# Optimization experiments

Measured on AMD Instinct MI355X. Metric: run time of the kernel, lower is better.

The kernel has to match this reference:

```python
import jax, jax.numpy as jnp
import numpy as np

PART_INDICES = [[0, 1, 2, 3, 4], [5, 6, 11, 12], [5, 7, 9], [6, 8, 10], [11, 12, 13, 14, 15, 16]]
B, J, D_IN, D_H, D_OUT = 4096, 25, 512, 256, 512


def _xavier(key, shape):
    fan_in, fan_out = shape
    lim = float(np.sqrt(6.0 / (fan_in + fan_out)))
    return jax.random.uniform(key, shape, jnp.float32, -lim, lim)


def setup_inputs() -> dict:
    key = jax.random.key(0)
    ks = list(jax.random.split(key, 64))
    it = iter(ks)
    inp = {}
    inp["x"] = jax.random.normal(next(it), (B, J, D_IN), jnp.float32)
    inp["adj_global"] = jax.random.uniform(next(it), (J, J), jnp.float32)
    for p, idx in enumerate(PART_INDICES):
        n = len(idx)
        inp[f"adj_local_{p}"] = jax.random.uniform(next(it), (n, n), jnp.float32)
    # global GCN params (2 layers)
    inp["Wg0"] = _xavier(next(it), (D_IN, D_H)); inp["bg0"] = jnp.zeros((D_H,), jnp.float32)
    inp["Wg1"] = _xavier(next(it), (D_H, D_OUT)); inp["bg1"] = jnp.zeros((D_OUT,), jnp.float32)
    # local GCN params (5 parts x 2 layers)
    for p in range(5):
        inp[f"Wl{p}a"] = _xavier(next(it), (D_IN, D_H)); inp[f"bl{p}a"] = jnp.zeros((D_H,), jnp.float32)
        inp[f"Wl{p}b"] = _xavier(next(it), (D_H, D_OUT)); inp[f"bl{p}b"] = jnp.zeros((D_OUT,), jnp.float32)
    # fusion MLP: Linear(2*D_OUT, D_OUT) -> ReLU -> Linear(D_OUT, D_OUT)
    inp["Wf0"] = _xavier(next(it), (2 * D_OUT, D_OUT)); inp["bf0"] = jnp.zeros((D_OUT,), jnp.float32)
    inp["Wf1"] = _xavier(next(it), (D_OUT, D_OUT)); inp["bf1"] = jnp.zeros((D_OUT,), jnp.float32)
    return inp


def _gcn(x, adj, W, b):
    # symmetric degree normalization D^-1/2 A D^-1/2, then (norm_adj @ (x @ W)) + b
    d = jnp.clip(adj.sum(axis=1), 1e-6, None) ** -0.5
    norm_adj = d[:, None] * adj * d[None, :]                       # [n, n]
    return jnp.einsum('ij,bjf->bif', norm_adj, x @ W) + b          # [B, n, out]


def reference(x, adj_global, adj_local_0, adj_local_1, adj_local_2, adj_local_3, adj_local_4,
              Wg0, bg0, Wg1, bg1,
              Wl0a, bl0a, Wl0b, bl0b,
              Wl1a, bl1a, Wl1b, bl1b,
              Wl2a, bl2a, Wl2b, bl2b,
              Wl3a, bl3a, Wl3b, bl3b,
              Wl4a, bl4a, Wl4b, bl4b,
              Wf0, bf0, Wf1, bf1):
    adjs = [adj_local_0, adj_local_1, adj_local_2, adj_local_3, adj_local_4]
    lps = [(Wl0a, bl0a, Wl0b, bl0b), (Wl1a, bl1a, Wl1b, bl1b), (Wl2a, bl2a, Wl2b, bl2b),
           (Wl3a, bl3a, Wl3b, bl3b), (Wl4a, bl4a, Wl4b, bl4b)]
    # global branch
    xg = jax.nn.relu(_gcn(x, adj_global, Wg0, bg0))
    xg = jax.nn.relu(_gcn(xg, adj_global, Wg1, bg1))
    # local branch: scatter per-part outputs back (later parts overwrite overlaps, like torch)
    xl = jnp.zeros((x.shape[0], x.shape[1], D_OUT), x.dtype)
    for p, idx in enumerate(PART_INDICES):
        Wa, ba, Wb, bb = lps[p]
        idx_a = jnp.asarray(idx)
        xp = x[:, idx_a]                                           # [B, n_p, D_IN]
        xp = jax.nn.relu(_gcn(xp, adjs[p], Wa, ba))
        xp = jax.nn.relu(_gcn(xp, adjs[p], Wb, bb))
        xl = xl.at[:, idx_a].set(xp)
    # fusion MLP
    xc = jnp.concatenate([xg, xl], axis=-1)                        # [B, J, 2*D_OUT]
    return jax.nn.relu(xc @ Wf0 + bf0) @ Wf1 + bf1                 # [B, J, D_OUT]
```

## Files before the change

kernel.cpp:

```cpp
#include <hip/hip_runtime.h>


#define BATCH 4096
#define NJOINT 25
#define MROWS (BATCH * NJOINT)
#define SZ_FULL (MROWS * 512)

typedef __attribute__((ext_vector_type(8))) short short8;
typedef __attribute__((ext_vector_type(4))) float float4_;

__device__ __forceinline__ float b2f(ushort u) {
    union { float f; uint32_t i; } x; x.i = ((uint32_t)u) << 16; return x.f;
}
__device__ __forceinline__ ushort f2b(float f) {
    union { float f; uint32_t i; } x; x.f = f;
    uint32_t r = x.i + 0x7fff + ((x.i >> 16) & 1);
    return (ushort)(r >> 16);
}
__device__ __forceinline__ void async16(const void* g, void* l) {
    __builtin_amdgcn_global_load_lds(
        (const __attribute__((address_space(1))) void*)g,
        (__attribute__((address_space(3))) void*)l, 16, 0, 0);
}

__device__ void norm_one(const float* A, int n, float* out, float* sAdj, float* sD) {
    int t = threadIdx.x;
    for (int i = t; i < n * n; i += 256) sAdj[i] = A[i];
    __syncthreads();
    if (t < n) {
        float s = 0.f;
        for (int j = 0; j < n; j++) s += sAdj[t * n + j];
        sD[t] = 1.0f / sqrtf(fmaxf(s, 1e-6f));
    }
    __syncthreads();
    for (int i = t; i < n * n; i += 256) {
        int r = i / n, c = i % n;
        out[i] = sD[r] * sAdj[i] * sD[c];
    }
    __syncthreads();
}

__global__ __launch_bounds__(256) void adjnorm_kernel(
    const float* Ag, const float* A0, const float* A2, const float* A3,
    const float* A4, float* ADJ) {
    __shared__ float sAdj[640];
    __shared__ float sD[32];
    norm_one(Ag, 25, ADJ, sAdj, sD);
    norm_one(A0, 5, ADJ + 640 + 0 * 64, sAdj, sD);
    norm_one(A2, 3, ADJ + 640 + 1 * 64, sAdj, sD);
    norm_one(A3, 3, ADJ + 640 + 2 * 64, sAdj, sD);
    norm_one(A4, 6, ADJ + 640 + 3 * 64, sAdj, sD);
}

__global__ __launch_bounds__(256) void cvt_bf16(const float* __restrict__ in,
                                                ushort* __restrict__ out, int n4) {
    int id = blockIdx.x * 256 + threadIdx.x;
    if (id < n4) {
        float4 v = ((const float4*)in)[id];
        ushort4 o;
        o.x = f2b(v.x); o.y = f2b(v.y); o.z = f2b(v.z); o.w = f2b(v.w);
        ((ushort4*)out)[id] = o;
    }
}

struct WDesc { const float* W; ushort* Wt; int K, N, nxlog, end; };
struct WParams { WDesc d[12]; };

__global__ __launch_bounds__(256) void wtrans_all(WParams P) {
    __shared__ float tile[32][33];
    int bid = blockIdx.x;
    int i = 0, start = 0;
    while (bid >= P.d[i].end) { start = P.d[i].end; i++; }
    const WDesc& D = P.d[i];
    int local = bid - start;
    int bx = local & ((1 << D.nxlog) - 1);
    int by = local >> D.nxlog;
    int K = D.K, N = D.N;
    int t = threadIdx.x, tx = t & 31, ty = t >> 5;
    int k0 = by * 32, n0 = bx * 32;
    for (int r = ty; r < 32; r += 8)
        tile[r][tx] = D.W[(size_t)(k0 + r) * N + n0 + tx];
    __syncthreads();
    for (int r = ty; r < 32; r += 8)
        D.Wt[(size_t)(n0 + r) * K + k0 + tx] = f2b(tile[tx][r]);
}

__global__ __launch_bounds__(256) void zero_tail(ushort* __restrict__ XGL) {
    int id = blockIdx.x * 256 + threadIdx.x;
    int f4 = id & 127;
    int rj = (id >> 7) & 7;
    int b = id >> 10;
    ushort4 z; z.x = 0; z.y = 0; z.z = 0; z.w = 0;
    ((ushort4*)(XGL + ((size_t)(b * 25 + 17 + rj) * 1024 + 512)))[f4] = z;
}

struct GDesc {
    const ushort* A; const ushort* Wt; const float* bias; void* C;
    int K, lda, ldc, nTiles, wgEnd, gn, flags, pad;
    int gmap[6];
};
struct GParams { GDesc g[5]; };

__global__ __launch_bounds__(512, 2) void gemmg(GParams P) {
    __shared__ ushort lds[65536];
    int t = threadIdx.x;
    int l = t & 63, w = t >> 6;

    int nwg = (int)gridDim.x;
    int cpx = nwg >> 3;
    int wg = ((int)blockIdx.x & 7) * cpx + ((int)blockIdx.x >> 3);

    int gi = 0, wg0 = 0;
    while (wg >= P.g[gi].wgEnd) { wg0 = P.g[gi].wgEnd; gi++; }
    const GDesc& G = P.g[gi];
    int lw = wg - wg0;
    int tm, tn;
    if (G.nTiles == 2) { tm = lw >> 1; tn = lw & 1; }
    else               { tm = lw;      tn = 0; }
    int bm = tm << 8, bn = tn << 8;
    const int K = G.K, lda = G.lda, ldc = G.ldc;
    const bool GATHER = (G.flags & 1) != 0;
    const bool BIAS   = (G.flags & 2) != 0;
    const bool RELU   = (G.flags & 4) != 0;
    const bool OUTF32 = (G.flags & 8) != 0;

    int srow = (w << 4) + (l >> 3);
    int sch = ((l & 7) ^ (l >> 3)) << 3;
    const ushort* pA[2][2];
    const ushort* pB[2][2];
#pragma unroll
    for (int h = 0; h < 2; h++)
#pragma unroll
        for (int i = 0; i < 2; i++) {
            int r = bm + h * 128 + srow + i * 8;
            if (GATHER) { int b = r / G.gn; r = b * 25 + G.gmap[r - b * G.gn]; }
            pA[h][i] = G.A + (size_t)r * lda + sch;
            int c = bn + h * 128 + srow + i * 8;
            pB[h][i] = G.Wt + (size_t)c * K + sch;
        }
    int stga = w << 10;

    int wm = w >> 2, wn = w & 3;
    int lr = l & 15, q = l >> 4;
    int cx = lr & 7;
    int ca0 = (q ^ cx) << 3;
    int ca1 = ca0 ^ 32;
    int ra = (wm << 13) + (lr << 6);
    int rb = 16384 + ((wn >> 1) << 13) + ((wn & 1) << 12) + (lr << 6);

    float4_ acc[8][4];
#pragma unroll
    for (int fi = 0; fi < 8; fi++)
#pragma unroll
        for (int fj = 0; fj < 4; fj++) acc[fi][fj] = (float4_)0.f;
    short8 bfr[4][2];

#define FENCE() asm volatile("" ::: "memory")
#define STG_A(DB, H, KT) do {                                              \
        async16(pA[H][0] + (KT) * 64, &lds[(DB) + (H) * 8192 + stga]);     \
        async16(pA[H][1] + (KT) * 64, &lds[(DB) + (H) * 8192 + stga + 512]); \
    } while (0)
#define STG_B(DB, H, KT) do {                                              \
        async16(pB[H][0] + (KT) * 64, &lds[(DB) + 16384 + (H) * 8192 + stga]); \
        async16(pB[H][1] + (KT) * 64, &lds[(DB) + 16384 + (H) * 8192 + stga + 512]); \
    } while (0)

#define DO_PHASE(DB, FI0, RDB, WAITST, STMT) do {                          \
        short8 af00, af01, af10, af11;                                     \
        if (RDB) {                                                         \
            _Pragma("unroll")                                              \
            for (int fj = 0; fj < 4; fj++) {                               \
                bfr[fj][0] = *(const short8*)&lds[(DB) + rb + fj * 1024 + ca0]; \
                bfr[fj][1] = *(const short8*)&lds[(DB) + rb + fj * 1024 + ca1]; \
            }                                                              \
        }                                                                  \
        af00 = *(const short8*)&lds[(DB) + ra + (FI0) * 1024 + ca0];       \
        af01 = *(const short8*)&lds[(DB) + ra + (FI0) * 1024 + ca1];       \
        af10 = *(const short8*)&lds[(DB) + ra + ((FI0) + 1) * 1024 + ca0]; \
        af11 = *(const short8*)&lds[(DB) + ra + ((FI0) + 1) * 1024 + ca1]; \
        STMT                                                               \
        WAITST                                                             \
        __builtin_amdgcn_s_barrier();                                      \
        FENCE();                                                           \
        __builtin_amdgcn_s_setprio(1);                                     \
        _Pragma("unroll")                                                  \
        for (int fj = 0; fj < 4; fj++) {                                   \
            acc[FI0][fj] = __builtin_amdgcn_mfma_f32_16x16x32_bf16(        \
                af00, bfr[fj][0], acc[FI0][fj], 0, 0, 0);                  \
            acc[FI0][fj] = __builtin_amdgcn_mfma_f32_16x16x32_bf16(        \
                af01, bfr[fj][1], acc[FI0][fj], 0, 0, 0);                  \
            acc[(FI0) + 1][fj] = __builtin_amdgcn_mfma_f32_16x16x32_bf16(  \
                af10, bfr[fj][0], acc[(FI0) + 1][fj], 0, 0, 0);            \
            acc[(FI0) + 1][fj] = __builtin_amdgcn_mfma_f32_16x16x32_bf16(  \
                af11, bfr[fj][1], acc[(FI0) + 1][fj], 0, 0, 0);            \
        }                                                                  \
        __builtin_amdgcn_s_setprio(0);                                     \
        __builtin_amdgcn_s_barrier();                                      \
        FENCE();                                                           \
    } while (0)

    int NT = K >> 6;
    int NITER = NT >> 1;

    STG_A(0, 0, 0); STG_A(0, 1, 0);
    STG_B(0, 0, 0); STG_B(0, 1, 0);
    STG_B(32768, 0, 1); STG_B(32768, 1, 1);
    asm volatile("s_waitcnt vmcnt(4)" ::: "memory");
    __builtin_amdgcn_s_barrier();
    FENCE();

    for (int j = 0; j < NITER; ++j) {
        int k1 = 2 * j + 1, k2 = 2 * j + 2, k3 = 2 * j + 3;
        bool nl = (j + 1 < NITER);
        DO_PHASE(0, 0, true, , STG_A(32768, 0, k1););
        DO_PHASE(0, 2, false, , STG_A(32768, 1, k1););
        DO_PHASE(0, 4, false, , if (nl) STG_B(0, 0, k2););
        DO_PHASE(0, 6, false,
                 if (nl) { asm volatile("s_waitcnt vmcnt(4)" ::: "memory"); }
                 else    { asm volatile("s_waitcnt vmcnt(0)" ::: "memory"); },
                 if (nl) STG_B(0, 1, k2););
        DO_PHASE(32768, 0, true, , if (nl) STG_A(0, 0, k2););
        DO_PHASE(32768, 2, false, , if (nl) STG_A(0, 1, k2););
        DO_PHASE(32768, 4, false, , if (nl) STG_B(32768, 0, k3););
        DO_PHASE(32768, 6, false,
                 if (nl) { asm volatile("s_waitcnt vmcnt(4)" ::: "memory"); },
                 if (nl) STG_B(32768, 1, k3););
    }
#undef DO_PHASE
#undef STG_A
#undef STG_B
#undef FENCE

    int cl = lr;
    float bv[4];
#pragma unroll
    for (int fj = 0; fj < 4; fj++)
        bv[fj] = BIAS ? G.bias[bn + (wn << 6) + (fj << 4) + cl] : 0.f;
#pragma unroll
    for (int fi = 0; fi < 8; fi++) {
        int row0 = bm + (wm << 7) + (fi << 4) + (q << 2);
#pragma unroll
        for (int r = 0; r < 4; r++) {
            size_t rowoff = (size_t)(row0 + r) * ldc;
#pragma unroll
            for (int fj = 0; fj < 4; fj++) {
                int col = bn + (wn << 6) + (fj << 4) + cl;
                float v = acc[fi][fj][r] + bv[fj];
                if (RELU) v = fmaxf(v, 0.f);
                if (OUTF32)
                    ((float*)G.C)[rowoff + col] = v;
                else
                    ((ushort*)G.C)[rowoff + col] = f2b(v);
            }
        }
    }
}

struct M1Desc { ushort* T; const float* adj; const float* bias; int nj; };
struct M1Params { M1Desc d[5]; };

template <int NJ>
__device__ __forceinline__ void mix1_body(ushort* base, const float* As, float bi) {
    float v[NJ];
#pragma unroll
    for (int j = 0; j < NJ; j++) v[j] = b2f(base[(size_t)j * 256]);
#pragma unroll
    for (int i = 0; i < NJ; i++) {
        float o = 0.f;
#pragma unroll
        for (int j = 0; j < NJ; j++) o += As[i * NJ + j] * v[j];
        base[(size_t)i * 256] = f2b(fmaxf(o + bi, 0.f));
    }
}

__global__ __launch_bounds__(256) void mixg1(M1Params P) {
    __shared__ float As[625];
    int r = blockIdx.x >> 12;
    const M1Desc& D = P.d[r];
    int t = threadIdx.x;
    int nj = D.nj;
    for (int i = t; i < nj * nj; i += 256) As[i] = D.adj[i];
    __syncthreads();
    int id = ((blockIdx.x & 4095) << 8) + t;
    int f = id & 255, b = id >> 8;
    ushort* base = D.T + ((size_t)b * nj) * 256 + f;
    float bi = D.bias[f];
    switch (nj) {
        case 25: mix1_body<25>(base, As, bi); break;
        case 5:  mix1_body<5>(base, As, bi); break;
        case 3:  mix1_body<3>(base, As, bi); break;
        default: mix1_body<6>(base, As, bi); break;
    }
}

struct M2Desc {
    const ushort* src; ushort* dst; const float* adj; const float* bias;
    int nj, sldr; int jm[25];
};
struct M2Params { M2Desc d[5]; };

template <int NJ>
__device__ __forceinline__ void mix2_body(const ushort* src, int sldr, ushort* dst,
                                          const int* jms, const float* As, float bi) {
    float v[NJ];
#pragma unroll
    for (int j = 0; j < NJ; j++) v[j] = b2f(src[(size_t)j * sldr]);
#pragma unroll
    for (int i = 0; i < NJ; i++) {
        float o = 0.f;
#pragma unroll
        for (int j = 0; j < NJ; j++) o += As[i * NJ + j] * v[j];
        dst[(size_t)jms[i] * 1024] = f2b(fmaxf(o + bi, 0.f));
    }
}

__global__ __launch_bounds__(256) void mixg2(M2Params P) {
    __shared__ float As[625];
    __shared__ int jms[25];
    int r = blockIdx.x >> 13;
    const M2Desc& D = P.d[r];
    int t = threadIdx.x;
    int nj = D.nj;
    for (int i = t; i < nj * nj; i += 256) As[i] = D.adj[i];
    if (t < nj) jms[t] = D.jm[t];
    __syncthreads();
    int id = ((blockIdx.x & 8191) << 8) + t;
    int f = id & 511, b = id >> 9;
    const ushort* src = D.src + ((size_t)b * nj) * D.sldr + f;
    ushort* dst = D.dst + (size_t)b * 25 * 1024 + f;
    float bi = D.bias[f];
    switch (nj) {
        case 25: mix2_body<25>(src, D.sldr, dst, jms, As, bi); break;
        case 5:  mix2_body<5>(src, D.sldr, dst, jms, As, bi); break;
        case 3:  mix2_body<3>(src, D.sldr, dst, jms, As, bi); break;
        default: mix2_body<6>(src, D.sldr, dst, jms, As, bi); break;
    }
}

extern "C" void kernel_launch(void* const* d_in, const int* in_sizes, int n_in,
                              void* d_out, int out_size, void* d_ws,
                              size_t ws_size, hipStream_t stream) {
    const float* x    = (const float*)d_in[0];
    const float* adjg = (const float*)d_in[1];
    const float* al0  = (const float*)d_in[2];
    const float* al2  = (const float*)d_in[4];
    const float* al3  = (const float*)d_in[5];
    const float* al4  = (const float*)d_in[6];
    const float* Wg0  = (const float*)d_in[7];
    const float* bg0  = (const float*)d_in[8];
    const float* Wg1  = (const float*)d_in[9];
    const float* bg1  = (const float*)d_in[10];
    const float* Wf0  = (const float*)d_in[31];
    const float* bf0  = (const float*)d_in[32];
    const float* Wf1  = (const float*)d_in[33];
    const float* bf1  = (const float*)d_in[34];

    float* ws = (float*)d_ws;
    float* ADJ = ws;
    ushort* U   = (ushort*)(ws + 4096);
    ushort* Xb  = U;
    ushort* XGL = Xb + (size_t)SZ_FULL;
    ushort* T   = XGL + (size_t)MROWS * 1024;
    ushort* P1  = T + (size_t)MROWS * 256;
    ushort* Wb  = P1 + (size_t)BATCH * 17 * 256;
    ushort* P3  = Xb;
    ushort* HF  = Xb;

    ushort* Wg0t = Wb;
    ushort* Wg1t = Wb + 131072;
    ushort* Wf0t = Wb + 262144;
    ushort* Wf1t = Wb + 786432;
    ushort* Wpt  = Wb + 1048576;

    struct Part { int n, widx; int idx[6]; };
    const Part parts[4] = {
        {5, 11, {0, 1, 2, 3, 4, 0}},
        {3, 19, {5, 7, 9, 0, 0, 0}},
        {3, 23, {6, 8, 10, 0, 0, 0}},
        {6, 27, {11, 12, 13, 14, 15, 16}},
    };
    const int cumn[4] = {0, 5, 8, 11};

    dim3 blk(256), blk512(512);

    adjnorm_kernel<<<1, blk, 0, stream>>>(adjg, al0, al2, al3, al4, ADJ);
    cvt_bf16<<<SZ_FULL / 4 / 256, blk, 0, stream>>>(x, Xb, SZ_FULL / 4);
    zero_tail<<<16384, blk, 0, stream>>>(XGL);

    {
        WParams WP{};
        int e = 0, i = 0;
        auto add = [&](const float* W, ushort* Wt, int K, int N) {
            int nx = N >> 5;
            int nxlog = (nx == 8) ? 3 : ((nx == 16) ? 4 : 5);
            e += nx * (K >> 5);
            WP.d[i++] = {W, Wt, K, N, nxlog, e};
        };
        add(Wg0, Wg0t, 512, 256);
        add(Wg1, Wg1t, 256, 512);
        add(Wf0, Wf0t, 1024, 512);
        add(Wf1, Wf1t, 512, 512);
        for (int qv = 0; qv < 4; qv++) {
            add((const float*)d_in[parts[qv].widx], Wpt + qv * 262144, 512, 256);
            add((const float*)d_in[parts[qv].widx + 2], Wpt + qv * 262144 + 131072, 256, 512);
        }
        wtrans_all<<<2048, blk, 0, stream>>>(WP);
    }

    auto setg = [](GDesc& g, const ushort* A, const ushort* Wt, const float* bias,
                   void* C, int K, int lda, int ldc, int nT, int wgEnd, int gn,
                   int flags, const int* map) {
        g.A = A; g.Wt = Wt; g.bias = bias; g.C = C; g.K = K; g.lda = lda;
        g.ldc = ldc; g.nTiles = nT; g.wgEnd = wgEnd; g.gn = gn; g.flags = flags;
        g.pad = 0;
        for (int i = 0; i < 6; i++) g.gmap[i] = map ? map[i] : 0;
    };

    {
        GParams GA{};
        int e = 400;
        setg(GA.g[0], Xb, Wg0t, nullptr, T, 512, 512, 256, 1, e, 0, 0, nullptr);
        for (int qv = 0; qv < 4; qv++) {
            e += parts[qv].n * 16;
            setg(GA.g[1 + qv], Xb, Wpt + qv * 262144, nullptr,
                 P1 + (size_t)BATCH * cumn[qv] * 256,
                 512, 512, 256, 1, e, parts[qv].n, 1, parts[qv].idx);
        }
        gemmg<<<672, blk512, 0, stream>>>(GA);
    }

    {
        M1Params M1{};
        M1.d[0] = {T, ADJ, bg0, 25};
        for (int qv = 0; qv < 4; qv++)
            M1.d[1 + qv] = {P1 + (size_t)BATCH * cumn[qv] * 256,
                            ADJ + 640 + qv * 64,
                            (const float*)d_in[parts[qv].widx + 1],
                            parts[qv].n};
        mixg1<<<20480, blk, 0, stream>>>(M1);
    }

    {
        GParams GB{};
        int e = 800;
        setg(GB.g[0], T, Wg1t, nullptr, XGL, 256, 256, 1024, 2, e, 0, 0, nullptr);
        for (int qv = 0; qv < 4; qv++) {
            e += parts[qv].n * 32;
            setg(GB.g[1 + qv], P1 + (size_t)BATCH * cumn[qv] * 256,
                 Wpt + qv * 262144 + 131072, nullptr,
                 P3 + (size_t)BATCH * cumn[qv] * 512,
                 256, 256, 512, 2, e, 0, 0, nullptr);
        }
        gemmg<<<1344, blk512, 0, stream>>>(GB);
    }

    {
        M2Params M2{};
        M2.d[0].src = XGL; M2.d[0].dst = XGL; M2.d[0].adj = ADJ;
        M2.d[0].bias = bg1; M2.d[0].nj = 25; M2.d[0].sldr = 1024;
        for (int i = 0; i < 25; i++) M2.d[0].jm[i] = i;
        for (int qv = 0; qv < 4; qv++) {
            M2Desc& D = M2.d[1 + qv];
            D.src = P3 + (size_t)BATCH * cumn[qv] * 512;
            D.dst = XGL + 512;
            D.adj = ADJ + 640 + qv * 64;
            D.bias = (const float*)d_in[parts[qv].widx + 3];
            D.nj = parts[qv].n; D.sldr = 512;
            for (int i = 0; i < 25; i++) D.jm[i] = (i < 6) ? parts[qv].idx[i] : 0;
        }
        mixg2<<<40960, blk, 0, stream>>>(M2);
    }

    {
        GParams GF{};
        setg(GF.g[0], XGL, Wf0t, bf0, HF, 1024, 1024, 512, 2, 800, 0, 2 | 4, nullptr);
        gemmg<<<800, blk512, 0, stream>>>(GF);
    }
    {
        GParams GO{};
        setg(GO.g[0], HF, Wf1t, bf1, d_out, 512, 512, 512, 2, 800, 0, 2 | 8, nullptr);
        gemmg<<<800, blk512, 0, stream>>>(GO);
    }

    (void)in_sizes; (void)n_in; (void)out_size; (void)ws_size;
}
```

Before: 963.9 us.

## Halve GEMM pipeline phases to four per iteration with explicit lgkmcnt waits

Restructures the double-buffered MFMA main loop so each phase computes four row fragments (32 MFMAs) instead of two. The phase count per k-pair drops from eight to four, and the number of workgroup barriers falls with it. Each phase now issues four async global-to-LDS loads instead of two. Explicit lgkmcnt waits and sched_barriers replace the compiler memory fences to control where LDS reads overlap the barrier. This trades finer load/compute interleaving and some register pressure for less synchronization overhead, and the vmcnt accounting has to stay consistent with the new load grouping.

```diff
diff --git a/kernel.cpp b/kernel.cpp
--- a/kernel.cpp
+++ b/kernel.cpp
@@ -155,18 +155,21 @@
         for (int fj = 0; fj < 4; fj++) acc[fi][fj] = (float4_)0.f;
     short8 bfr[4][2];
 
-#define FENCE() asm volatile("" ::: "memory")
-#define STG_A(DB, H, KT) do {                                              \
-        async16(pA[H][0] + (KT) * 64, &lds[(DB) + (H) * 8192 + stga]);     \
-        async16(pA[H][1] + (KT) * 64, &lds[(DB) + (H) * 8192 + stga + 512]); \
+#define STG_AT(DB, KT) do {                                                \
+        async16(pA[0][0] + (KT) * 64, &lds[(DB) + stga]);                  \
+        async16(pA[0][1] + (KT) * 64, &lds[(DB) + stga + 512]);            \
+        async16(pA[1][0] + (KT) * 64, &lds[(DB) + 8192 + stga]);           \
+        async16(pA[1][1] + (KT) * 64, &lds[(DB) + 8192 + stga + 512]);     \
     } while (0)
-#define STG_B(DB, H, KT) do {                                              \
-        async16(pB[H][0] + (KT) * 64, &lds[(DB) + 16384 + (H) * 8192 + stga]); \
-        async16(pB[H][1] + (KT) * 64, &lds[(DB) + 16384 + (H) * 8192 + stga + 512]); \
+#define STG_BT(DB, KT) do {                                                \
+        async16(pB[0][0] + (KT) * 64, &lds[(DB) + 16384 + stga]);          \
+        async16(pB[0][1] + (KT) * 64, &lds[(DB) + 16384 + stga + 512]);    \
+        async16(pB[1][0] + (KT) * 64, &lds[(DB) + 24576 + stga]);          \
+        async16(pB[1][1] + (KT) * 64, &lds[(DB) + 24576 + stga + 512]);    \
     } while (0)
 
 #define DO_PHASE(DB, FI0, RDB, WAITST, STMT) do {                          \
-        short8 af00, af01, af10, af11;                                     \
+        short8 af[4][2];                                                   \
         if (RDB) {                                                         \
             _Pragma("unroll")                                              \
             for (int fj = 0; fj < 4; fj++) {                               \
@@ -174,62 +177,58 @@
                 bfr[fj][1] = *(const short8*)&lds[(DB) + rb + fj * 1024 + ca1]; \
             }                                                              \
         }                                                                  \
-        af00 = *(const short8*)&lds[(DB) + ra + (FI0) * 1024 + ca0];       \
-        af01 = *(const short8*)&lds[(DB) + ra + (FI0) * 1024 + ca1];       \
-        af10 = *(const short8*)&lds[(DB) + ra + ((FI0) + 1) * 1024 + ca0]; \
-        af11 = *(const short8*)&lds[(DB) + ra + ((FI0) + 1) * 1024 + ca1]; \
+        _Pragma("unroll")                                                  \
+        for (int fi = 0; fi < 4; fi++) {                                   \
+            af[fi][0] = *(const short8*)&lds[(DB) + ra + ((FI0) + fi) * 1024 + ca0]; \
+            af[fi][1] = *(const short8*)&lds[(DB) + ra + ((FI0) + fi) * 1024 + ca1]; \
+        }                                                                  \
         STMT                                                               \
         WAITST                                                             \
+        if (RDB) asm volatile("s_waitcnt lgkmcnt(8)");                     \
+        __builtin_amdgcn_sched_barrier(0);                                 \
         __builtin_amdgcn_s_barrier();                                      \
-        FENCE();                                                           \
+        asm volatile("s_waitcnt lgkmcnt(0)" ::: "memory");                 \
+        __builtin_amdgcn_sched_barrier(0);                                 \
         __builtin_amdgcn_s_setprio(1);                                     \
         _Pragma("unroll")                                                  \
-        for (int fj = 0; fj < 4; fj++) {                                   \
-            acc[FI0][fj] = __builtin_amdgcn_mfma_f32_16x16x32_bf16(        \
-                af00, bfr[fj][0], acc[FI0][fj], 0, 0, 0);                  \
-            acc[FI0][fj] = __builtin_amdgcn_mfma_f32_16x16x32_bf16(        \
-                af01, bfr[fj][1], acc[FI0][fj], 0, 0, 0);                  \
-            acc[(FI0) + 1][fj] = __builtin_amdgcn_mfma_f32_16x16x32_bf16(  \
-                af10, bfr[fj][0], acc[(FI0) + 1][fj], 0, 0, 0);            \
-            acc[(FI0) + 1][fj] = __builtin_amdgcn_mfma_f32_16x16x32_bf16(  \
-                af11, bfr[fj][1], acc[(FI0) + 1][fj], 0, 0, 0);            \
-        }                                                                  \
+        for (int kk = 0; kk < 2; kk++)                                     \
+            _Pragma("unroll")                                              \
+            for (int fi = 0; fi < 4; fi++)                                 \
+                _Pragma("unroll")                                          \
+                for (int fj = 0; fj < 4; fj++)                             \
+                    acc[(FI0) + fi][fj] = __builtin_amdgcn_mfma_f32_16x16x32_bf16( \
+                        af[fi][kk], bfr[fj][kk], acc[(FI0) + fi][fj], 0, 0, 0); \
         __builtin_amdgcn_s_setprio(0);                                     \
+        __builtin_amdgcn_sched_barrier(0);                                 \
         __builtin_amdgcn_s_barrier();                                      \
-        FENCE();                                                           \
     } while (0)
 
     int NT = K >> 6;
     int NITER = NT >> 1;
 
-    STG_A(0, 0, 0); STG_A(0, 1, 0);
-    STG_B(0, 0, 0); STG_B(0, 1, 0);
-    STG_B(32768, 0, 1); STG_B(32768, 1, 1);
+    STG_AT(0, 0);
+    STG_BT(0, 0);
+    STG_BT(32768, 1);
     asm volatile("s_waitcnt vmcnt(4)" ::: "memory");
+    __builtin_amdgcn_sched_barrier(0);
     __builtin_amdgcn_s_barrier();
-    FENCE();
 
     for (int j = 0; j < NITER; ++j) {
         int k1 = 2 * j + 1, k2 = 2 * j + 2, k3 = 2 * j + 3;
         bool nl = (j + 1 < NITER);
-        DO_PHASE(0, 0, true, , STG_A(32768, 0, k1););
-        DO_PHASE(0, 2, false, , STG_A(32768, 1, k1););
-        DO_PHASE(0, 4, false, , if (nl) STG_B(0, 0, k2););
-        DO_PHASE(0, 6, false,
+        DO_PHASE(0, 0, true, , STG_AT(32768, k1););
+        DO_PHASE(0, 4, false,
                  if (nl) { asm volatile("s_waitcnt vmcnt(4)" ::: "memory"); }
                  else    { asm volatile("s_waitcnt vmcnt(0)" ::: "memory"); },
-                 if (nl) STG_B(0, 1, k2););
-        DO_PHASE(32768, 0, true, , if (nl) STG_A(0, 0, k2););
-        DO_PHASE(32768, 2, false, , if (nl) STG_A(0, 1, k2););
-        DO_PHASE(32768, 4, false, , if (nl) STG_B(32768, 0, k3););
-        DO_PHASE(32768, 6, false,
+                 if (nl) STG_BT(0, k2););
+        DO_PHASE(32768, 0, true, , if (nl) STG_AT(0, k2););
+        DO_PHASE(32768, 4, false,
                  if (nl) { asm volatile("s_waitcnt vmcnt(4)" ::: "memory"); },
-                 if (nl) STG_B(32768, 1, k3););
+                 if (nl) STG_BT(32768, k3););
     }
 #undef DO_PHASE
-#undef STG_A
-#undef STG_B
-#undef FENCE
+#undef STG_AT
+#undef STG_BT
 
     int cl = lr;
     float bv[4];
```

Result: slower. 1.020 ms (+5.8%).
